# Kernel tuning notes

Measured on AMD Instinct MI355X. Metric: run time of the kernel, lower is better.

Reference implementation:

```python
import jax, jax.numpy as jnp
import numpy as np

N = 100000      # nodes
E = 1250000     # edges
IN = 128        # in_channels
H = 64          # hidden_channels
L = 2           # num_layers (GCNConv count)
EPS = 1e-5      # BatchNorm eps


def setup_inputs() -> dict:
    key = jax.random.key(0)
    ks = jax.random.split(key, 10)
    x = jax.random.normal(ks[0], (N, IN), jnp.float32)
    edge_index = jax.random.randint(ks[1], (2, E), 0, N, dtype=jnp.int32)
    fc_w = jax.random.normal(ks[2], (IN, H), jnp.float32) / np.sqrt(IN)
    fc_b = jax.random.normal(ks[3], (H,), jnp.float32) * 0.01
    conv_w = jax.random.normal(ks[4], (L, H, H), jnp.float32) / np.sqrt(H)
    conv_b = jax.random.normal(ks[5], (L, H), jnp.float32) * 0.01
    bn_gamma = jnp.ones((L + 1, H), jnp.float32)
    bn_beta = jnp.zeros((L + 1, H), jnp.float32)
    bn_mean = jax.random.normal(ks[6], (L + 1, H), jnp.float32) * 0.1
    bn_var = jax.random.uniform(ks[7], (L + 1, H), jnp.float32) + 0.5
    return {"x": x, "edge_index": edge_index, "fc_w": fc_w, "fc_b": fc_b,
            "conv_w": conv_w, "conv_b": conv_b, "bn_gamma": bn_gamma,
            "bn_beta": bn_beta, "bn_mean": bn_mean, "bn_var": bn_var}


def reference(x, edge_index, fc_w, fc_b, conv_w, conv_b, bn_gamma, bn_beta, bn_mean, bn_var):
    n = x.shape[0]
    loops = jnp.arange(n, dtype=edge_index.dtype)
    src = jnp.concatenate([edge_index[0], loops])   # add self-loops (GCNConv default)
    dst = jnp.concatenate([edge_index[1], loops])
    # symmetric normalization: deg computed on destination, norm = d_s^-1/2 * d_d^-1/2
    deg = jax.ops.segment_sum(jnp.ones_like(dst, x.dtype), dst, num_segments=n)
    dis = jax.lax.rsqrt(deg)                        # deg >= 1 thanks to self-loops
    norm = dis[src] * dis[dst]                      # [E+N]

    def bn(h, i):  # eval-mode BatchNorm1d with running stats
        return (h - bn_mean[i]) * (bn_gamma[i] * jax.lax.rsqrt(bn_var[i] + EPS)) + bn_beta[i]

    h = jax.nn.relu(bn(x @ fc_w + fc_b, 0))         # [N, H]; dropout is identity in eval
    last = h
    for i in range(conv_w.shape[0]):
        hw = h @ conv_w[i]                          # GCNConv: transform then aggregate
        agg = jax.ops.segment_sum(hw[src] * norm[:, None], dst, num_segments=n) + conv_b[i]
        h = jax.nn.relu(bn(agg, i + 1)) + last      # residual to post-fc activation
    return h
```

## Files before the change

kernel.cpp:

```cpp
#include <hip/hip_runtime.h>

#define NNODES 100000
#define NEDGES 1250000
#define IN_CH 128
#define HID 64
#define BN_EPS 1e-5f

#define NPAD 100352
#define DRANGE 12500
#define BIN_CHUNK 2048
#define BIN_BLOCKS 611
#define BIN_CAP_LDS 384
#define BIN_REGION 312500
#define FILL_BLOCKS 512
#define GBLOCKS 3125
#define ELL_C 32
#define OVF_CAP 65536

typedef __attribute__((ext_vector_type(8))) short s16x8;
typedef __attribute__((ext_vector_type(4))) float f32x4;

__device__ __forceinline__ ushort f2bf(float f) {
    union { float f; unsigned int i; } c;
    c.f = f;
    unsigned int lsb = (c.i >> 16) & 1u;
    return (ushort)((c.i + 0x7FFFu + lsb) >> 16);
}
__device__ __forceinline__ float bf2f(ushort u) {
    union { unsigned int i; float f; } c;
    c.i = (unsigned int)u << 16;
    return c.f;
}
__device__ __forceinline__ float asf(unsigned int i) {
    union { unsigned int i; float f; } c;
    c.i = i;
    return c.f;
}

__device__ __forceinline__ void fill_direct(int d, int soff, int* cnt,
                                            int* ell, int* ovf_n, int2* ovf) {
    int slot = atomicAdd(&cnt[d], 1);
    if (slot < ELL_C) ell[(d << 5) + slot] = soff;
    else {
        int oi = atomicAdd(ovf_n, 1);
        if (oi < OVF_CAP) ovf[oi] = make_int2(d, soff);
    }
}

__global__ __launch_bounds__(256) void edge_bin(
        const int* __restrict__ src, const int* __restrict__ dst,
        unsigned int* __restrict__ staged, int* bin_n,
        int* cnt, int* __restrict__ ell, int* ovf_n, int2* __restrict__ ovf) {
    __shared__ unsigned int sbin[8][BIN_CAP_LDS];
    __shared__ int scnt[8];
    __shared__ int sbase[8];
    const int tid = threadIdx.x;
    if (tid < 8) scnt[tid] = 0;
    __syncthreads();

    const int base = blockIdx.x * (BIN_CHUNK / 4);
    const int4* dst4 = (const int4*)dst;
    const int4* src4 = (const int4*)src;
#pragma unroll
    for (int k = 0; k < BIN_CHUNK / 1024; ++k) {
        int i = base + k * 256 + tid;
        if (i < NEDGES / 4) {
            int4 dv = dst4[i];
            int4 sv = src4[i];
#define BIN_ONE(D, S)                                                       \
            {                                                               \
                int b_ = (D) / DRANGE;                                      \
                unsigned int pk_ = ((unsigned int)((D) - b_ * DRANGE) << 17)\
                                   | (unsigned int)(S);                     \
                int sl_ = atomicAdd(&scnt[b_], 1);                          \
                if (sl_ < BIN_CAP_LDS) sbin[b_][sl_] = pk_;                 \
                else fill_direct((D), (S) << 7, cnt, ell, ovf_n, ovf);      \
            }
            BIN_ONE(dv.x, sv.x)
            BIN_ONE(dv.y, sv.y)
            BIN_ONE(dv.z, sv.z)
            BIN_ONE(dv.w, sv.w)
#undef BIN_ONE
        }
    }
    __syncthreads();
    if (tid < 8) {
        int c = scnt[tid];
        if (c > BIN_CAP_LDS) c = BIN_CAP_LDS;
        sbase[tid] = atomicAdd(&bin_n[tid], c);
    }
    __syncthreads();
#pragma unroll
    for (int b = 0; b < 8; ++b) {
        int c = scnt[b];
        if (c > BIN_CAP_LDS) c = BIN_CAP_LDS;
        int gb = sbase[b];
        for (int i = tid; i < c; i += 256) {
            int g = gb + i;
            unsigned int v = sbin[b][i];
            if (g < BIN_REGION) {
                staged[(size_t)b * BIN_REGION + g] = v;
            } else {
                int d = b * DRANGE + (int)(v >> 17);
                fill_direct(d, (int)(v & 0x1FFFFu) << 7, cnt, ell, ovf_n, ovf);
            }
        }
    }
}

__global__ __launch_bounds__(256) void ell_fill(
        const unsigned int* __restrict__ staged, const int* __restrict__ bin_n,
        int* cnt, int* __restrict__ ell, int* ovf_n, int2* __restrict__ ovf) {
    const int p  = blockIdx.x & 7;
    const int bi = blockIdx.x >> 3;
    const int nb = FILL_BLOCKS / 8;
    int n = bin_n[p];
    if (n > BIN_REGION) n = BIN_REGION;
    const unsigned int* sp = staged + (size_t)p * BIN_REGION;
    const int lo = p * DRANGE;
    for (int i = bi * 256 + threadIdx.x; i < n; i += nb * 256) {
        unsigned int v = sp[i];
        int d = lo + (int)(v >> 17);
        int soff = (int)(v & 0x1FFFFu) << 7;
        int slot = atomicAdd(&cnt[d], 1);
        if (slot < ELL_C) ell[(d << 5) + slot] = soff;
        else {
            int oi = atomicAdd(ovf_n, 1);
            if (oi < OVF_CAP) ovf[oi] = make_int2(d, soff);
        }
    }
}

__global__ __launch_bounds__(256) void fc_bn_relu(
        const float* __restrict__ x, const float* __restrict__ w,
        const float* __restrict__ b,
        const float* __restrict__ g, const float* __restrict__ be,
        const float* __restrict__ mu, const float* __restrict__ var,
        const int* __restrict__ cnt, float* __restrict__ dis,
        ushort* __restrict__ h0) {
    const int wave = threadIdx.x >> 6;
    const int lane = threadIdx.x & 63;
    const int m = lane & 15;
    const int q = lane >> 4;
    const int node_base = (blockIdx.x * 4 + wave) * 16;

    if (m == 0) {
#pragma unroll
        for (int r = 0; r < 4; ++r) {
            int node = node_base + q * 4 + r;
            if (node < NNODES) dis[node] = rsqrtf((float)(cnt[node] + 1));
        }
    }

    s16x8 bfrag[4][4];
#pragma unroll
    for (int kc = 0; kc < 4; ++kc)
#pragma unroll
        for (int ct = 0; ct < 4; ++ct)
#pragma unroll
            for (int j = 0; j < 8; ++j)
                bfrag[kc][ct][j] = (short)f2bf(w[(kc * 32 + q * 8 + j) * HID + ct * 16 + m]);

    f32x4 acc[4] = {{0,0,0,0},{0,0,0,0},{0,0,0,0},{0,0,0,0}};

    int row = node_base + m;
    if (row >= NNODES) row = NNODES - 1;
    const float4* xp = (const float4*)(x + (size_t)row * IN_CH + q * 8);

#pragma unroll
    for (int kc = 0; kc < 4; ++kc) {
        float4 a0 = xp[kc * 8 + 0];
        float4 a1 = xp[kc * 8 + 1];
        s16x8 af;
        af[0] = (short)f2bf(a0.x); af[1] = (short)f2bf(a0.y);
        af[2] = (short)f2bf(a0.z); af[3] = (short)f2bf(a0.w);
        af[4] = (short)f2bf(a1.x); af[5] = (short)f2bf(a1.y);
        af[6] = (short)f2bf(a1.z); af[7] = (short)f2bf(a1.w);
#pragma unroll
        for (int ct = 0; ct < 4; ++ct)
            acc[ct] = __builtin_amdgcn_mfma_f32_16x16x32_bf16(af, bfrag[kc][ct], acc[ct], 0, 0, 0);
    }

#pragma unroll
    for (int ct = 0; ct < 4; ++ct) {
        int col = ct * 16 + m;
        float sc = g[col] * rsqrtf(var[col] + BN_EPS);
        float off = (b[col] - mu[col]) * sc + be[col];
#pragma unroll
        for (int r = 0; r < 4; ++r) {
            int node = node_base + q * 4 + r;
            if (node < NNODES)
                h0[(size_t)node * HID + col] =
                    f2bf(fmaxf(acc[ct][r] * sc + off, 0.f));
        }
    }
}

__global__ __launch_bounds__(256) void conv_mm(
        const ushort* __restrict__ h, const float* __restrict__ w,
        const float* __restrict__ dis, ushort* __restrict__ hws) {
    const int wave = threadIdx.x >> 6;
    const int lane = threadIdx.x & 63;
    const int m = lane & 15;
    const int q = lane >> 4;
    const int node_base = (blockIdx.x * 4 + wave) * 16;

    s16x8 bfrag[2][4];
#pragma unroll
    for (int kc = 0; kc < 2; ++kc)
#pragma unroll
        for (int ct = 0; ct < 4; ++ct)
#pragma unroll
            for (int j = 0; j < 8; ++j)
                bfrag[kc][ct][j] = (short)f2bf(w[(kc * 32 + q * 8 + j) * HID + ct * 16 + m]);

    f32x4 acc[4] = {{0,0,0,0},{0,0,0,0},{0,0,0,0},{0,0,0,0}};

    int row = node_base + m;
    if (row >= NNODES) row = NNODES - 1;

#pragma unroll
    for (int kc = 0; kc < 2; ++kc) {
        const s16x8* hp = (const s16x8*)(h + (size_t)row * HID + kc * 32 + q * 8);
        s16x8 af = *hp;
#pragma unroll
        for (int ct = 0; ct < 4; ++ct)
            acc[ct] = __builtin_amdgcn_mfma_f32_16x16x32_bf16(af, bfrag[kc][ct], acc[ct], 0, 0, 0);
    }

    float dv[4];
#pragma unroll
    for (int r = 0; r < 4; ++r) {
        int node = node_base + q * 4 + r;
        dv[r] = (node < NNODES) ? dis[node] : 0.f;
    }
#pragma unroll
    for (int ct = 0; ct < 4; ++ct) {
#pragma unroll
        for (int r = 0; r < 4; ++r) {
            int node = node_base + q * 4 + r;
            if (node < NNODES)
                hws[(size_t)node * HID + ct * 16 + m] = f2bf(acc[ct][r] * dv[r]);
        }
    }
}

__global__ __launch_bounds__(256) void gather_update(
        const ushort* __restrict__ hws,
        const int* __restrict__ cnt, const int* __restrict__ ell,
        const int* __restrict__ ovf_n, const int2* __restrict__ ovf,
        const float* __restrict__ dis,
        const float* __restrict__ bias,
        const float* __restrict__ g, const float* __restrict__ be,
        const float* __restrict__ mu, const float* __restrict__ var,
        const ushort* __restrict__ last,
        ushort* __restrict__ out_bf, float* __restrict__ out_f,
        int write_f32) {
    const int wave = threadIdx.x >> 6;
    const int lane = threadIdx.x & 63;
    const int grp  = lane >> 3;
    const int j    = lane & 7;
    const int d = blockIdx.x * 32 + wave * 8 + grp;
    const unsigned int moff = (unsigned int)j * 16u;
    const unsigned int doff = ((unsigned int)d << 7) + moff;

    const char* hb = (const char*)hws;

    float a[8];
    {
        uint4 sv = *(const uint4*)(hb + doff);
        a[0] = asf(sv.x << 16); a[1] = asf(sv.x & 0xffff0000u);
        a[2] = asf(sv.y << 16); a[3] = asf(sv.y & 0xffff0000u);
        a[4] = asf(sv.z << 16); a[5] = asf(sv.z & 0xffff0000u);
        a[6] = asf(sv.w << 16); a[7] = asf(sv.w & 0xffff0000u);
    }

#define ACC8(V)                                                         \
    a[0] += asf((V).x << 16); a[1] += asf((V).x & 0xffff0000u);         \
    a[2] += asf((V).y << 16); a[3] += asf((V).y & 0xffff0000u);         \
    a[4] += asf((V).z << 16); a[5] += asf((V).z & 0xffff0000u);         \
    a[6] += asf((V).w << 16); a[7] += asf((V).w & 0xffff0000u);

    const int n = cnt[d];
    const int nn = (n < ELL_C) ? n : ELL_C;
    const int* sp = ell + ((size_t)d << 5);

    int k = 0;
    for (; k + 8 <= nn; k += 8) {
        unsigned int o0 = (unsigned int)sp[k + 0] + moff;
        unsigned int o1 = (unsigned int)sp[k + 1] + moff;
        unsigned int o2 = (unsigned int)sp[k + 2] + moff;
        unsigned int o3 = (unsigned int)sp[k + 3] + moff;
        unsigned int o4 = (unsigned int)sp[k + 4] + moff;
        unsigned int o5 = (unsigned int)sp[k + 5] + moff;
        unsigned int o6 = (unsigned int)sp[k + 6] + moff;
        unsigned int o7 = (unsigned int)sp[k + 7] + moff;
        uint4 v0 = *(const uint4*)(hb + o0);
        uint4 v1 = *(const uint4*)(hb + o1);
        uint4 v2 = *(const uint4*)(hb + o2);
        uint4 v3 = *(const uint4*)(hb + o3);
        uint4 v4 = *(const uint4*)(hb + o4);
        uint4 v5 = *(const uint4*)(hb + o5);
        uint4 v6 = *(const uint4*)(hb + o6);
        uint4 v7 = *(const uint4*)(hb + o7);
        ACC8(v0) ACC8(v1) ACC8(v2) ACC8(v3)
        ACC8(v4) ACC8(v5) ACC8(v6) ACC8(v7)
    }
    for (; k + 4 <= nn; k += 4) {
        unsigned int o0 = (unsigned int)sp[k + 0] + moff;
        unsigned int o1 = (unsigned int)sp[k + 1] + moff;
        unsigned int o2 = (unsigned int)sp[k + 2] + moff;
        unsigned int o3 = (unsigned int)sp[k + 3] + moff;
        uint4 v0 = *(const uint4*)(hb + o0);
        uint4 v1 = *(const uint4*)(hb + o1);
        uint4 v2 = *(const uint4*)(hb + o2);
        uint4 v3 = *(const uint4*)(hb + o3);
        ACC8(v0) ACC8(v1) ACC8(v2) ACC8(v3)
    }
    for (; k < nn; ++k) {
        uint4 v = *(const uint4*)(hb + ((unsigned int)sp[k] + moff));
        ACC8(v)
    }
    if (n > ELL_C) {
        int on = *ovf_n;
        if (on > OVF_CAP) on = OVF_CAP;
        for (int jj = 0; jj < on; ++jj) {
            int2 e = ovf[jj];
            if (e.x == d) {
                uint4 v = *(const uint4*)(hb + ((unsigned int)e.y + moff));
                ACC8(v)
            }
        }
    }
#undef ACC8

    float dd = dis[d];
    float4 bi0 = ((const float4*)bias)[2 * j], bi1 = ((const float4*)bias)[2 * j + 1];
    float4 g0  = ((const float4*)g)[2 * j],    g1  = ((const float4*)g)[2 * j + 1];
    float4 be0 = ((const float4*)be)[2 * j],   be1 = ((const float4*)be)[2 * j + 1];
    float4 mu0 = ((const float4*)mu)[2 * j],   mu1 = ((const float4*)mu)[2 * j + 1];
    float4 va0 = ((const float4*)var)[2 * j],  va1 = ((const float4*)var)[2 * j + 1];
    uint4 lv = *(const uint4*)((const char*)last + doff);
    float l0 = asf(lv.x << 16), l1 = asf(lv.x & 0xffff0000u);
    float l2 = asf(lv.y << 16), l3 = asf(lv.y & 0xffff0000u);
    float l4 = asf(lv.z << 16), l5 = asf(lv.z & 0xffff0000u);
    float l6 = asf(lv.w << 16), l7 = asf(lv.w & 0xffff0000u);

#define EPI(A, BI, GV, BE, MU, VA, LO) \
    (fmaxf(((A) * dd + (BI) - (MU)) * ((GV) * rsqrtf((VA) + BN_EPS)) + (BE), 0.f) + (LO))
    float r0 = EPI(a[0], bi0.x, g0.x, be0.x, mu0.x, va0.x, l0);
    float r1 = EPI(a[1], bi0.y, g0.y, be0.y, mu0.y, va0.y, l1);
    float r2 = EPI(a[2], bi0.z, g0.z, be0.z, mu0.z, va0.z, l2);
    float r3 = EPI(a[3], bi0.w, g0.w, be0.w, mu0.w, va0.w, l3);
    float r4 = EPI(a[4], bi1.x, g1.x, be1.x, mu1.x, va1.x, l4);
    float r5 = EPI(a[5], bi1.y, g1.y, be1.y, mu1.y, va1.y, l5);
    float r6 = EPI(a[6], bi1.z, g1.z, be1.z, mu1.z, va1.z, l6);
    float r7 = EPI(a[7], bi1.w, g1.w, be1.w, mu1.w, va1.w, l7);
#undef EPI

    if (write_f32) {
        float4* op = (float4*)(out_f + (size_t)d * HID + j * 8);
        op[0] = make_float4(r0, r1, r2, r3);
        op[1] = make_float4(r4, r5, r6, r7);
    } else {
        uint4 o;
        o.x = (unsigned int)f2bf(r0) | ((unsigned int)f2bf(r1) << 16);
        o.y = (unsigned int)f2bf(r2) | ((unsigned int)f2bf(r3) << 16);
        o.z = (unsigned int)f2bf(r4) | ((unsigned int)f2bf(r5) << 16);
        o.w = (unsigned int)f2bf(r6) | ((unsigned int)f2bf(r7) << 16);
        *(uint4*)((char*)out_bf + doff) = o;
    }
}

extern "C" void kernel_launch(void* const* d_in, const int* in_sizes, int n_in,
                              void* d_out, int out_size, void* d_ws, size_t ws_size,
                              hipStream_t stream) {
    const float* x      = (const float*)d_in[0];
    const int*   eidx   = (const int*)d_in[1];
    const float* fc_w   = (const float*)d_in[2];
    const float* fc_b   = (const float*)d_in[3];
    const float* conv_w = (const float*)d_in[4];
    const float* conv_b = (const float*)d_in[5];
    const float* bn_g   = (const float*)d_in[6];
    const float* bn_b   = (const float*)d_in[7];
    const float* bn_m   = (const float*)d_in[8];
    const float* bn_v   = (const float*)d_in[9];

    const int* src = eidx;
    const int* dst = eidx + NEDGES;

    float* out = (float*)d_out;

    float*  dis     = (float*)d_ws;
    int*    cnt     = (int*)(dis + NPAD);
    int*    meta    = cnt + NPAD;
    int*    ovf_n   = meta;
    int*    bin_n   = meta + 8;
    int2*   ovf     = (int2*)(meta + 16);
    int*    ell     = (int*)(ovf + OVF_CAP);
    ushort* h0      = (ushort*)(ell + (size_t)NNODES * ELL_C);
    ushort* h1      = h0 + (size_t)NNODES * HID;
    ushort* hws     = h1 + (size_t)NNODES * HID;
    unsigned int* staged = (unsigned int*)hws;

    const int BLK = 256;
    const int gridMM  = (NNODES + 63) / 64;

    hipMemsetAsync(cnt, 0, (size_t)NPAD * 4 + 64, stream);

    edge_bin<<<BIN_BLOCKS, BLK, 0, stream>>>(src, dst, staged, bin_n,
                                             cnt, ell, ovf_n, ovf);
    ell_fill<<<FILL_BLOCKS, BLK, 0, stream>>>(staged, bin_n,
                                              cnt, ell, ovf_n, ovf);

    fc_bn_relu<<<gridMM, BLK, 0, stream>>>(x, fc_w, fc_b, bn_g, bn_b, bn_m, bn_v,
                                           cnt, dis, h0);

    conv_mm<<<gridMM, BLK, 0, stream>>>(h0, conv_w, dis, hws);
    gather_update<<<GBLOCKS, BLK, 0, stream>>>(hws, cnt, ell, ovf_n, ovf, dis,
                                               conv_b, bn_g + HID, bn_b + HID,
                                               bn_m + HID, bn_v + HID, h0,
                                               h1, nullptr, 0);

    conv_mm<<<gridMM, BLK, 0, stream>>>(h1, conv_w + HID * HID, dis, hws);
    gather_update<<<GBLOCKS, BLK, 0, stream>>>(hws, cnt, ell, ovf_n, ovf, dis,
                                               conv_b + HID, bn_g + 2 * HID, bn_b + 2 * HID,
                                               bn_m + 2 * HID, bn_v + 2 * HID, h0,
                                               nullptr, out, 1);
}
```

Before: 312.4 us.

## Refine edge binning to 256 narrow destination bins with one fill block per bin

Edge binning now uses 256 destination ranges of 391 nodes each instead of 8 ranges of 12500. Each ell_fill block then handles exactly one bin, so its count atomics and ELL writes stay within a small, cache-resident node range. The fill loop is also unrolled four ways to keep more loads in flight. In exchange, the per-block LDS bins are small (32 entries), so staging writes become shorter and more scattered, and the fill stage runs only 256 blocks.

Measured after the change: 295.0 us. 5.6% less time.

```diff
diff --git a/kernel.cpp b/kernel.cpp
--- a/kernel.cpp
+++ b/kernel.cpp
@@ -7,12 +7,12 @@
 #define BN_EPS 1e-5f
 
 #define NPAD 100352
-#define DRANGE 12500
+#define BIN_N 256
+#define BINW 391
 #define BIN_CHUNK 2048
 #define BIN_BLOCKS 611
-#define BIN_CAP_LDS 384
-#define BIN_REGION 312500
-#define FILL_BLOCKS 512
+#define BIN_CAP_LDS 32
+#define BIN_REGION 10000
 #define GBLOCKS 3125
 #define ELL_C 32
 #define OVF_CAP 65536
@@ -51,11 +51,11 @@
         const int* __restrict__ src, const int* __restrict__ dst,
         unsigned int* __restrict__ staged, int* bin_n,
         int* cnt, int* __restrict__ ell, int* ovf_n, int2* __restrict__ ovf) {
-    __shared__ unsigned int sbin[8][BIN_CAP_LDS];
-    __shared__ int scnt[8];
-    __shared__ int sbase[8];
+    __shared__ unsigned int sbin[BIN_N][BIN_CAP_LDS];
+    __shared__ int scnt[BIN_N];
+    __shared__ int sbase[BIN_N];
     const int tid = threadIdx.x;
-    if (tid < 8) scnt[tid] = 0;
+    scnt[tid] = 0;
     __syncthreads();
 
     const int base = blockIdx.x * (BIN_CHUNK / 4);
@@ -69,8 +69,8 @@
             int4 sv = src4[i];
 #define BIN_ONE(D, S)                                                       \
             {                                                               \
-                int b_ = (D) / DRANGE;                                      \
-                unsigned int pk_ = ((unsigned int)((D) - b_ * DRANGE) << 17)\
+                int b_ = (D) / BINW;                                        \
+                unsigned int pk_ = ((unsigned int)((D) - b_ * BINW) << 17)  \
                                    | (unsigned int)(S);                     \
                 int sl_ = atomicAdd(&scnt[b_], 1);                          \
                 if (sl_ < BIN_CAP_LDS) sbin[b_][sl_] = pk_;                 \
@@ -84,24 +84,24 @@
         }
     }
     __syncthreads();
-    if (tid < 8) {
+    {
         int c = scnt[tid];
         if (c > BIN_CAP_LDS) c = BIN_CAP_LDS;
         sbase[tid] = atomicAdd(&bin_n[tid], c);
     }
     __syncthreads();
-#pragma unroll
-    for (int b = 0; b < 8; ++b) {
+    const int wave = tid >> 6;
+    const int lane = tid & 63;
+    for (int b = wave; b < BIN_N; b += 4) {
         int c = scnt[b];
         if (c > BIN_CAP_LDS) c = BIN_CAP_LDS;
-        int gb = sbase[b];
-        for (int i = tid; i < c; i += 256) {
-            int g = gb + i;
-            unsigned int v = sbin[b][i];
+        if (lane < c) {
+            int g = sbase[b] + lane;
+            unsigned int v = sbin[b][lane];
             if (g < BIN_REGION) {
                 staged[(size_t)b * BIN_REGION + g] = v;
             } else {
-                int d = b * DRANGE + (int)(v >> 17);
+                int d = b * BINW + (int)(v >> 17);
                 fill_direct(d, (int)(v & 0x1FFFFu) << 7, cnt, ell, ovf_n, ovf);
             }
         }
@@ -111,23 +111,25 @@
 __global__ __launch_bounds__(256) void ell_fill(
         const unsigned int* __restrict__ staged, const int* __restrict__ bin_n,
         int* cnt, int* __restrict__ ell, int* ovf_n, int2* __restrict__ ovf) {
-    const int p  = blockIdx.x & 7;
-    const int bi = blockIdx.x >> 3;
-    const int nb = FILL_BLOCKS / 8;
-    int n = bin_n[p];
+    const int b = blockIdx.x;
+    int n = bin_n[b];
     if (n > BIN_REGION) n = BIN_REGION;
-    const unsigned int* sp = staged + (size_t)p * BIN_REGION;
-    const int lo = p * DRANGE;
-    for (int i = bi * 256 + threadIdx.x; i < n; i += nb * 256) {
+    const unsigned int* sp = staged + (size_t)b * BIN_REGION;
+    const int lo = b * BINW;
+    int i = threadIdx.x;
+    for (; i + 768 < n; i += 1024) {
+        unsigned int v0 = sp[i];
+        unsigned int v1 = sp[i + 256];
+        unsigned int v2 = sp[i + 512];
+        unsigned int v3 = sp[i + 768];
+        fill_direct(lo + (int)(v0 >> 17), (int)(v0 & 0x1FFFFu) << 7, cnt, ell, ovf_n, ovf);
+        fill_direct(lo + (int)(v1 >> 17), (int)(v1 & 0x1FFFFu) << 7, cnt, ell, ovf_n, ovf);
+        fill_direct(lo + (int)(v2 >> 17), (int)(v2 & 0x1FFFFu) << 7, cnt, ell, ovf_n, ovf);
+        fill_direct(lo + (int)(v3 >> 17), (int)(v3 & 0x1FFFFu) << 7, cnt, ell, ovf_n, ovf);
+    }
+    for (; i < n; i += 256) {
         unsigned int v = sp[i];
-        int d = lo + (int)(v >> 17);
-        int soff = (int)(v & 0x1FFFFu) << 7;
-        int slot = atomicAdd(&cnt[d], 1);
-        if (slot < ELL_C) ell[(d << 5) + slot] = soff;
-        else {
-            int oi = atomicAdd(ovf_n, 1);
-            if (oi < OVF_CAP) ovf[oi] = make_int2(d, soff);
-        }
+        fill_direct(lo + (int)(v >> 17), (int)(v & 0x1FFFFu) << 7, cnt, ell, ovf_n, ovf);
     }
 }
 
@@ -395,8 +397,8 @@
     int*    cnt     = (int*)(dis + NPAD);
     int*    meta    = cnt + NPAD;
     int*    ovf_n   = meta;
-    int*    bin_n   = meta + 8;
-    int2*   ovf     = (int2*)(meta + 16);
+    int*    bin_n   = meta + 16;
+    int2*   ovf     = (int2*)(meta + 272);
     int*    ell     = (int*)(ovf + OVF_CAP);
     ushort* h0      = (ushort*)(ell + (size_t)NNODES * ELL_C);
     ushort* h1      = h0 + (size_t)NNODES * HID;
@@ -406,12 +408,12 @@
     const int BLK = 256;
     const int gridMM  = (NNODES + 63) / 64;
 
-    hipMemsetAsync(cnt, 0, (size_t)NPAD * 4 + 64, stream);
+    hipMemsetAsync(cnt, 0, (size_t)NPAD * 4 + 272 * 4, stream);
 
     edge_bin<<<BIN_BLOCKS, BLK, 0, stream>>>(src, dst, staged, bin_n,
                                              cnt, ell, ovf_n, ovf);
-    ell_fill<<<FILL_BLOCKS, BLK, 0, stream>>>(staged, bin_n,
-                                              cnt, ell, ovf_n, ovf);
+    ell_fill<<<BIN_N, BLK, 0, stream>>>(staged, bin_n,
+                                        cnt, ell, ovf_n, ovf);
 
     fc_bn_relu<<<gridMM, BLK, 0, stream>>>(x, fc_w, fc_b, bn_g, bn_b, bn_m, bn_v,
                                            cnt, dis, h0);
```
